# Optimization experiments

Measured on AMD Instinct MI355X. Metric: run time of the kernel, lower is better.

The kernel has to match this reference:

```python
import jax, jax.numpy as jnp
import numpy as np

N_NODES = 1048576
N_EDGES = 16777216
N_GRAPHS = 64
K_HOPS = 4


def setup_inputs() -> dict:
    key = jax.random.key(0)
    k1, k2, k3 = jax.random.split(key, 3)
    x = jax.random.normal(k1, (N_NODES, 1), dtype=jnp.float32)
    edge_index = jax.random.randint(k2, (2, N_EDGES), 0, N_NODES, dtype=jnp.int64)
    W = jax.random.normal(k3, (1, 1), dtype=jnp.float32)
    b = jnp.zeros((1,), dtype=jnp.float32)
    return {"x": x, "edge_index": edge_index, "W": W, "b": b, "num_graphs": N_GRAPHS}


def _sgconv(x, edge_index, W, b, k):
    # PyG SGConv: x <- (D^-1/2 (A + I) D^-1/2)^k x, then linear.
    n = x.shape[0]
    loops = jnp.arange(n, dtype=edge_index.dtype)
    row = jnp.concatenate([edge_index[0], loops])  # source nodes
    col = jnp.concatenate([edge_index[1], loops])  # target nodes
    ones = jnp.ones(row.shape[0], dtype=x.dtype)
    deg = jax.ops.segment_sum(ones, col, num_segments=n)  # in-degree incl. self loop
    dinv = jnp.where(deg > 0, jax.lax.rsqrt(deg), 0.0)
    norm = dinv[row] * dinv[col]  # [E+N]
    for _ in range(k):
        x = jax.ops.segment_sum(norm[:, None] * x[row], col, num_segments=n)
    return x @ W.T + b


def reference(x, edge_index, W, b, num_graphs):
    h = _sgconv(x, edge_index, W, b, K_HOPS)  # [N, 1]
    n = h.shape[0]
    # tensor_split into num_graphs equal chunks (N divisible by num_graphs), mean each
    out = h.reshape(num_graphs, n // num_graphs, 1).mean(axis=1)  # [B, 1]
    return out
```

## Files before the change

### kernel.cpp

```cpp
#include <hip/hip_runtime.h>
#include <stdint.h>

#define N_NODES  (1u << 20)
#define N_EDGES  (1u << 24)
#define N_GRAPHS 64
#define CHUNK    (N_NODES / N_GRAPHS)
#define K_HOPS   4

#define NBUCKET  1024
#define CPB      1024
#define CAP      18432

#define NBLK_SS  512
#define TB_SS    1024
#define EPT      32
#define EPB_SS   (TB_SS * EPT)

typedef uint32_t u32x4 __attribute__((ext_vector_type(4)));
typedef unsigned long long u64x2 __attribute__((ext_vector_type(2)));

__device__ __forceinline__ u32x4 nt_load_u32x4(const uint32_t* p) {
    return __builtin_nontemporal_load((const u32x4*)p);
}
__device__ __forceinline__ u64x2 nt_load_u64x2(const unsigned long long* p) {
    return __builtin_nontemporal_load((const u64x2*)p);
}

__global__ __launch_bounds__(TB_SS, 4)
void scatter_sort_kernel(const void* __restrict__ ei,
                         int* __restrict__ cursor, uint32_t* __restrict__ packed) {
    __shared__ uint32_t sorted[EPB_SS];
    __shared__ int h[NBUCKET];
    __shared__ int o[NBUCKET];
    __shared__ int ostart[NBUCKET];
    __shared__ int gbase[NBUCKET];
    __shared__ int s_is64;
    int blk = blockIdx.x, tid = threadIdx.x;
    h[tid] = 0;
    size_t base = (size_t)blk * EPB_SS;

    if (tid < 64) {
        size_t widx = 2 * base + 2 * (size_t)tid * 512 + 1;
        int nz = (((const uint32_t*)ei)[widx] != 0u);
        unsigned long long m = __ballot(nz);
        if (tid == 0) s_is64 = (m == 0ull) ? 1 : 0;
    }
    __syncthreads();
    int is64 = s_is64;
    uint32_t c_[EPT];

    if (is64) {
        const unsigned long long* cp = (const unsigned long long*)ei + N_EDGES + base;
        #pragma unroll
        for (int it = 0; it < EPT / 4; ++it) {
            size_t i = (size_t)it * (TB_SS * 4) + (size_t)tid * 4;
            u64x2 a = nt_load_u64x2(cp + i);
            u64x2 b2 = nt_load_u64x2(cp + i + 2);
            c_[it * 4 + 0] = (uint32_t)a.x;  c_[it * 4 + 1] = (uint32_t)a.y;
            c_[it * 4 + 2] = (uint32_t)b2.x; c_[it * 4 + 3] = (uint32_t)b2.y;
            atomicAdd(&h[c_[it * 4 + 0] >> 10], 1);
            atomicAdd(&h[c_[it * 4 + 1] >> 10], 1);
            atomicAdd(&h[c_[it * 4 + 2] >> 10], 1);
            atomicAdd(&h[c_[it * 4 + 3] >> 10], 1);
        }
    } else {
        const uint32_t* cp = (const uint32_t*)ei + N_EDGES + base;
        #pragma unroll
        for (int it = 0; it < EPT / 4; ++it) {
            size_t i = (size_t)it * (TB_SS * 4) + (size_t)tid * 4;
            u32x4 a = nt_load_u32x4(cp + i);
            c_[it * 4 + 0] = a.x; c_[it * 4 + 1] = a.y;
            c_[it * 4 + 2] = a.z; c_[it * 4 + 3] = a.w;
            atomicAdd(&h[a.x >> 10], 1);
            atomicAdd(&h[a.y >> 10], 1);
            atomicAdd(&h[a.z >> 10], 1);
            atomicAdd(&h[a.w >> 10], 1);
        }
    }
    __syncthreads();

    if (tid < 64) {
        int b16 = tid * 16;
        int s = 0;
        #pragma unroll
        for (int j = 0; j < 16; ++j) s += h[b16 + j];
        int v = s;
        #pragma unroll
        for (int off = 1; off < 64; off <<= 1) {
            int up = __shfl_up(v, off, 64);
            if (tid >= off) v += up;
        }
        int run = v - s;
        #pragma unroll
        for (int j = 0; j < 16; ++j) {
            o[b16 + j] = run;
            ostart[b16 + j] = run;
            run += h[b16 + j];
        }
    }
    __syncthreads();

    gbase[tid] = atomicAdd(&cursor[tid], h[tid]);

    if (is64) {
        const unsigned long long* rp = (const unsigned long long*)ei + base;
        #pragma unroll
        for (int it = 0; it < EPT / 4; ++it) {
            size_t i = (size_t)it * (TB_SS * 4) + (size_t)tid * 4;
            u64x2 a = nt_load_u64x2(rp + i);
            u64x2 b2 = nt_load_u64x2(rp + i + 2);
            uint32_t r0 = (uint32_t)a.x, r1 = (uint32_t)a.y;
            uint32_t r2 = (uint32_t)b2.x, r3 = (uint32_t)b2.y;
            { uint32_t c = c_[it * 4 + 0]; int pos = atomicAdd(&o[c >> 10], 1); sorted[pos] = (r0 << 10) | (c & 1023u); }
            { uint32_t c = c_[it * 4 + 1]; int pos = atomicAdd(&o[c >> 10], 1); sorted[pos] = (r1 << 10) | (c & 1023u); }
            { uint32_t c = c_[it * 4 + 2]; int pos = atomicAdd(&o[c >> 10], 1); sorted[pos] = (r2 << 10) | (c & 1023u); }
            { uint32_t c = c_[it * 4 + 3]; int pos = atomicAdd(&o[c >> 10], 1); sorted[pos] = (r3 << 10) | (c & 1023u); }
        }
    } else {
        const uint32_t* rp = (const uint32_t*)ei + base;
        #pragma unroll
        for (int it = 0; it < EPT / 4; ++it) {
            size_t i = (size_t)it * (TB_SS * 4) + (size_t)tid * 4;
            u32x4 a = nt_load_u32x4(rp + i);
            { uint32_t c = c_[it * 4 + 0]; int pos = atomicAdd(&o[c >> 10], 1); sorted[pos] = (a.x << 10) | (c & 1023u); }
            { uint32_t c = c_[it * 4 + 1]; int pos = atomicAdd(&o[c >> 10], 1); sorted[pos] = (a.y << 10) | (c & 1023u); }
            { uint32_t c = c_[it * 4 + 2]; int pos = atomicAdd(&o[c >> 10], 1); sorted[pos] = (a.z << 10) | (c & 1023u); }
            { uint32_t c = c_[it * 4 + 3]; int pos = atomicAdd(&o[c >> 10], 1); sorted[pos] = (a.w << 10) | (c & 1023u); }
        }
    }
    __syncthreads();

    int wave = tid >> 6, lane = tid & 63;
    for (int k = 0; k < NBUCKET / 16; ++k) {
        int b = wave * (NBUCKET / 16) + k;
        int st = ostart[b];
        int len = o[b] - st;
        int gb = gbase[b];
        if (gb + len > CAP) len = CAP - gb > 0 ? CAP - gb : 0;
        uint32_t* dst = packed + (size_t)b * CAP + gb;
        for (int j = lane; j < len; j += 64)
            dst[j] = sorted[st + j];
    }
}

__global__ __launch_bounds__(512)
void degdinv_kernel(const uint32_t* __restrict__ packed, const int* __restrict__ cursor,
                    const float* __restrict__ x,
                    float* __restrict__ dinv, float* __restrict__ z) {
    __shared__ int h[CPB];
    int b = blockIdx.x, tid = threadIdx.x;
    for (int l = tid; l < CPB; l += 512) h[l] = 0;
    __syncthreads();
    int cnt = cursor[b]; if (cnt > CAP) cnt = CAP;
    const uint32_t* seg = packed + (size_t)b * CAP;
    int nq = cnt >> 2;
    for (int g = tid; g < nq; g += 512) {
        u32x4 v = nt_load_u32x4(seg + g * 4);
        atomicAdd(&h[v.x & 1023u], 1);
        atomicAdd(&h[v.y & 1023u], 1);
        atomicAdd(&h[v.z & 1023u], 1);
        atomicAdd(&h[v.w & 1023u], 1);
    }
    int t = (nq << 2) + tid;
    if (t < cnt) atomicAdd(&h[seg[t] & 1023u], 1);
    __syncthreads();
    for (int l = tid; l < CPB; l += 512) {
        int v = b * CPB + l;
        float d = (float)(1.0 / sqrt((double)(h[l] + 1)));
        dinv[v] = d;
        z[v] = d * x[v];
    }
}

__global__ __launch_bounds__(512)
void hop_kernel(const uint32_t* __restrict__ packed, const int* __restrict__ cursor,
                const float* __restrict__ z, const float* __restrict__ dinv,
                float* __restrict__ out) {
    __shared__ float facc[CPB];
    int b = blockIdx.x, tid = threadIdx.x;
    for (int l = tid; l < CPB; l += 512) facc[l] = 0.0f;
    __syncthreads();
    int cnt = cursor[b]; if (cnt > CAP) cnt = CAP;
    const uint32_t* seg = packed + (size_t)b * CAP;
    int nq = cnt >> 2;
    for (int g = tid; g < nq; g += 512) {
        u32x4 v = nt_load_u32x4(seg + g * 4);
        float z0 = z[v.x >> 10];
        float z1 = z[v.y >> 10];
        float z2 = z[v.z >> 10];
        float z3 = z[v.w >> 10];
        atomicAdd(&facc[v.x & 1023u], z0);
        atomicAdd(&facc[v.y & 1023u], z1);
        atomicAdd(&facc[v.z & 1023u], z2);
        atomicAdd(&facc[v.w & 1023u], z3);
    }
    int t = (nq << 2) + tid;
    if (t < cnt) { uint32_t p = seg[t]; atomicAdd(&facc[p & 1023u], z[p >> 10]); }
    __syncthreads();
    for (int l = tid; l < CPB; l += 512) {
        int v = b * CPB + l;
        float tt = z[v] + facc[l];
        float d = dinv[v];
        out[v] = d * d * tt;
    }
}

__global__ __launch_bounds__(512)
void hop_final_kernel(const uint32_t* __restrict__ packed, const int* __restrict__ cursor,
                      const float* __restrict__ z, const float* __restrict__ dinv,
                      float* __restrict__ gsum) {
    __shared__ float facc[CPB];
    __shared__ double sdata[8];
    int b = blockIdx.x, tid = threadIdx.x;
    for (int l = tid; l < CPB; l += 512) facc[l] = 0.0f;
    __syncthreads();
    int cnt = cursor[b]; if (cnt > CAP) cnt = CAP;
    const uint32_t* seg = packed + (size_t)b * CAP;
    int nq = cnt >> 2;
    for (int g = tid; g < nq; g += 512) {
        u32x4 v = nt_load_u32x4(seg + g * 4);
        float z0 = z[v.x >> 10];
        float z1 = z[v.y >> 10];
        float z2 = z[v.z >> 10];
        float z3 = z[v.w >> 10];
        atomicAdd(&facc[v.x & 1023u], z0);
        atomicAdd(&facc[v.y & 1023u], z1);
        atomicAdd(&facc[v.z & 1023u], z2);
        atomicAdd(&facc[v.w & 1023u], z3);
    }
    int t = (nq << 2) + tid;
    if (t < cnt) { uint32_t p = seg[t]; atomicAdd(&facc[p & 1023u], z[p >> 10]); }
    __syncthreads();
    double s = 0.0;
    for (int l = tid; l < CPB; l += 512) {
        int v = b * CPB + l;
        s += (double)(dinv[v] * (z[v] + facc[l]));
    }
    #pragma unroll
    for (int off = 32; off > 0; off >>= 1) s += __shfl_down(s, off, 64);
    int wave = tid >> 6, lane = tid & 63;
    if (lane == 0) sdata[wave] = s;
    __syncthreads();
    if (tid == 0) {
        double tot = 0.0;
        #pragma unroll
        for (int w = 0; w < 8; ++w) tot += sdata[w];
        atomicAdd(&gsum[b >> 4], (float)tot);
    }
}

__global__ void finalize_kernel(const float* __restrict__ gsum,
                                const float* __restrict__ W, const float* __restrict__ b,
                                float* __restrict__ out) {
    int g = threadIdx.x;
    if (g < N_GRAPHS)
        out[g] = (float)((double)W[0] * ((double)gsum[g] / (double)CHUNK) + (double)b[0]);
}

__global__ void detect_kernel(const uint32_t* __restrict__ ei, int* __restrict__ flag) {
    __shared__ int any_nz;
    if (threadIdx.x == 0) any_nz = 0;
    __syncthreads();
    int nz = 0;
    for (int i = threadIdx.x; i < 32768; i += blockDim.x)
        nz |= (ei[2 * i + 1] != 0u);
    if (nz) atomicOr(&any_nz, 1);
    __syncthreads();
    if (threadIdx.x == 0) flag[0] = any_nz ? 0 : 1;
}

__global__ void zero_int_kernel(int* __restrict__ p) {
    int i = blockIdx.x * blockDim.x + threadIdx.x;
    p[i] = 0;
}

__device__ __forceinline__ int load_idx(const void* ei, int is64, size_t pos) {
    if (is64) return (int)((const unsigned long long*)ei)[pos];
    return ((const int*)ei)[pos];
}

__global__ void count_kernel(const void* __restrict__ ei, const int* __restrict__ flag,
                             int* __restrict__ deg) {
    int e = blockIdx.x * blockDim.x + threadIdx.x;
    int c = load_idx(ei, flag[0], (size_t)N_EDGES + (size_t)e);
    atomicAdd(&deg[c], 1);
}

__global__ void dinv_kernel(const int* __restrict__ deg, float* __restrict__ dinv) {
    int v = blockIdx.x * blockDim.x + threadIdx.x;
    dinv[v] = (float)(1.0 / sqrt((double)(deg[v] + 1)));
}

__global__ void prep_first2_kernel(const float* __restrict__ x, const float* __restrict__ dinv,
                                   float* __restrict__ z, float* __restrict__ acc) {
    int v = blockIdx.x * blockDim.x + threadIdx.x;
    float t = dinv[v] * x[v];
    z[v] = t;
    acc[v] = t;
}

__global__ void prep_mid_kernel(const float* __restrict__ dinv,
                                float* __restrict__ z, float* __restrict__ acc) {
    int v = blockIdx.x * blockDim.x + threadIdx.x;
    float d = dinv[v];
    float t = d * d * acc[v];
    z[v] = t;
    acc[v] = t;
}

__global__ void push_kernel(const void* __restrict__ ei, const int* __restrict__ flag,
                            const float* __restrict__ z, float* __restrict__ acc) {
    int e = blockIdx.x * blockDim.x + threadIdx.x;
    int is64 = flag[0];
    int r, c;
    if (is64) {
        const unsigned long long* p = (const unsigned long long*)ei;
        r = (int)p[e];
        c = (int)p[(size_t)N_EDGES + (size_t)e];
    } else {
        const int* p = (const int*)ei;
        r = p[e];
        c = p[(size_t)N_EDGES + (size_t)e];
    }
    __hip_atomic_fetch_add(&acc[c], z[r], __ATOMIC_RELAXED, __HIP_MEMORY_SCOPE_AGENT);
}

__global__ void final_scale_kernel(const float* __restrict__ dinv,
                                   const float* __restrict__ acc, float* __restrict__ xf) {
    int v = blockIdx.x * blockDim.x + threadIdx.x;
    xf[v] = dinv[v] * acc[v];
}

__global__ void pool_kernel(const float* __restrict__ xf,
                            const float* __restrict__ W, const float* __restrict__ b,
                            float* __restrict__ out) {
    __shared__ double sdata[256];
    int g = blockIdx.x;
    int base = g * CHUNK;
    double s = 0.0;
    for (int i = threadIdx.x; i < CHUNK; i += 256) s += (double)xf[base + i];
    sdata[threadIdx.x] = s;
    __syncthreads();
    for (int off = 128; off > 0; off >>= 1) {
        if (threadIdx.x < off) sdata[threadIdx.x] += sdata[threadIdx.x + off];
        __syncthreads();
    }
    if (threadIdx.x == 0)
        out[g] = (float)((double)W[0] * (sdata[0] / (double)CHUNK) + (double)b[0]);
}

extern "C" void kernel_launch(void* const* d_in, const int* in_sizes, int n_in,
                              void* d_out, int out_size, void* d_ws, size_t ws_size,
                              hipStream_t stream) {
    const float* x = (const float*)d_in[0];
    const void*  ei = d_in[1];
    const float* W = (const float*)d_in[2];
    const float* b = (const float*)d_in[3];
    float* out = (float*)d_out;

    char* ws = (char*)d_ws;
    const size_t MB4 = 4ull << 20;
    size_t off_cursor = 0;
    size_t off_gsum   = NBUCKET * 4;
    size_t off_dinv   = off_gsum + 256;
    size_t off_za     = off_dinv + MB4;
    size_t off_zb     = off_za + MB4;
    size_t off_packed = off_zb + MB4;
    size_t needed     = off_packed + (size_t)NBUCKET * CAP * 4;

    const int TB = 256;

    if (ws_size >= needed) {
        int*      cursor = (int*)(ws + off_cursor);
        float*    gsum   = (float*)(ws + off_gsum);
        float*    dinv   = (float*)(ws + off_dinv);
        float*    za     = (float*)(ws + off_za);
        float*    zb     = (float*)(ws + off_zb);
        uint32_t* packed = (uint32_t*)(ws + off_packed);

        hipMemsetAsync(ws, 0, NBUCKET * 4 + 256, stream);

        scatter_sort_kernel<<<NBLK_SS, TB_SS, 0, stream>>>(ei, cursor, packed);
        degdinv_kernel<<<NBUCKET, 512, 0, stream>>>(packed, cursor, x, dinv, za);

        hop_kernel<<<NBUCKET, 512, 0, stream>>>(packed, cursor, za, dinv, zb);
        hop_kernel<<<NBUCKET, 512, 0, stream>>>(packed, cursor, zb, dinv, za);
        hop_kernel<<<NBUCKET, 512, 0, stream>>>(packed, cursor, za, dinv, zb);
        hop_final_kernel<<<NBUCKET, 512, 0, stream>>>(packed, cursor, zb, dinv, gsum);

        finalize_kernel<<<1, 64, 0, stream>>>(gsum, W, b, out);
    } else {
        int*   flag = (int*)ws;
        float* dinv = (float*)(ws + 256);
        float* za   = (float*)(ws + 256 + MB4);
        float* zb   = (float*)(ws + 256 + 2 * MB4);
        int*   deg  = (int*)(ws + 256 + 3 * MB4);

        detect_kernel<<<1, TB, 0, stream>>>((const uint32_t*)ei, flag);
        zero_int_kernel<<<N_NODES / TB, TB, 0, stream>>>(deg);
        count_kernel<<<N_EDGES / TB, TB, 0, stream>>>(ei, flag, deg);
        dinv_kernel<<<N_NODES / TB, TB, 0, stream>>>(deg, dinv);

        prep_first2_kernel<<<N_NODES / TB, TB, 0, stream>>>(x, dinv, za, zb);
        push_kernel<<<N_EDGES / TB, TB, 0, stream>>>(ei, flag, za, zb);
        for (int h = 1; h < K_HOPS; ++h) {
            prep_mid_kernel<<<N_NODES / TB, TB, 0, stream>>>(dinv, za, zb);
            push_kernel<<<N_EDGES / TB, TB, 0, stream>>>(ei, flag, za, zb);
        }
        final_scale_kernel<<<N_NODES / TB, TB, 0, stream>>>(dinv, zb, za);
        pool_kernel<<<N_GRAPHS, TB, 0, stream>>>(za, W, b, out);
    }
}
```

Measured before the change: 624.6 us.

## Tile edges by (target bucket, source shard) and row-sort tiles for z locality

Edges are now binned into 1024 tiles keyed by 64 target buckets of 16K nodes and 16 source shards of 64K nodes. A second pass sorts each tile by source row and builds global degrees, so the hop gathers read a 256KB slice of z in near-sequential order. Each hop accumulates 16K-wide partials in shared memory and atomically adds them to a global accumulator, followed by a separate merge kernel. The aim is better cache hit rates on the random z gathers, at the cost of an extra sort pass, global float atomics and extra merge launches per hop. Float atomic order is nondeterministic.

```diff
diff --git a/kernel.cpp b/kernel.cpp
--- a/kernel.cpp
+++ b/kernel.cpp
@@ -7,23 +7,318 @@
 #define CHUNK    (N_NODES / N_GRAPHS)
 #define K_HOPS   4
 
+#define NBLK_SS  1024
+#define TB_SS    1024
+#define EPT      16
+#define EPB_SS   (TB_SS * EPT)
+#define CAP      18432
+
 #define NBUCKET  1024
 #define CPB      1024
-#define CAP      18432
-
-#define NBLK_SS  512
-#define TB_SS    1024
-#define EPT      32
-#define EPB_SS   (TB_SS * EPT)
+
+#define NBKT2    64
+#define SHARDS   16
+#define NTILE    (NBKT2 * SHARDS)
+#define CPB2     16384
 
 typedef uint32_t u32x4 __attribute__((ext_vector_type(4)));
 typedef unsigned long long u64x2 __attribute__((ext_vector_type(2)));
+typedef float f32x4 __attribute__((ext_vector_type(4)));
+typedef int i32x4 __attribute__((ext_vector_type(4)));
 
 __device__ __forceinline__ u32x4 nt_load_u32x4(const uint32_t* p) {
     return __builtin_nontemporal_load((const u32x4*)p);
 }
 __device__ __forceinline__ u64x2 nt_load_u64x2(const unsigned long long* p) {
     return __builtin_nontemporal_load((const u64x2*)p);
+}
+__device__ __forceinline__ void nt_store_u32x4(uint32_t* p, u32x4 v) {
+    __builtin_nontemporal_store(v, (u32x4*)p);
+}
+
+__global__ __launch_bounds__(TB_SS, 4)
+void tile_sort_kernel(const void* __restrict__ ei,
+                      int* __restrict__ cursor, uint32_t* __restrict__ packed) {
+    __shared__ uint32_t sorted[EPB_SS];
+    __shared__ int h[NTILE];
+    __shared__ int o[NTILE];
+    __shared__ int ostart[NTILE];
+    __shared__ int gbase[NTILE];
+    __shared__ int s_is64;
+    int blk = blockIdx.x, tid = threadIdx.x;
+    h[tid] = 0;
+    size_t base = (size_t)blk * EPB_SS;
+
+    if (tid < 64) {
+        size_t widx = 2 * base + 2 * (size_t)tid * (EPB_SS / 64) + 1;
+        int nz = (((const uint32_t*)ei)[widx] != 0u);
+        unsigned long long m = __ballot(nz);
+        if (tid == 0) s_is64 = (m == 0ull) ? 1 : 0;
+    }
+    __syncthreads();
+    int is64 = s_is64;
+    uint32_t c_[EPT], r_[EPT];
+
+    if (is64) {
+        const unsigned long long* cp = (const unsigned long long*)ei + N_EDGES + base;
+        const unsigned long long* rp = (const unsigned long long*)ei + base;
+        #pragma unroll
+        for (int it = 0; it < EPT / 4; ++it) {
+            size_t i = (size_t)it * (TB_SS * 4) + (size_t)tid * 4;
+            u64x2 ca = nt_load_u64x2(cp + i);
+            u64x2 cb = nt_load_u64x2(cp + i + 2);
+            u64x2 ra = nt_load_u64x2(rp + i);
+            u64x2 rb = nt_load_u64x2(rp + i + 2);
+            c_[it * 4 + 0] = (uint32_t)ca.x;  c_[it * 4 + 1] = (uint32_t)ca.y;
+            c_[it * 4 + 2] = (uint32_t)cb.x;  c_[it * 4 + 3] = (uint32_t)cb.y;
+            r_[it * 4 + 0] = (uint32_t)ra.x;  r_[it * 4 + 1] = (uint32_t)ra.y;
+            r_[it * 4 + 2] = (uint32_t)rb.x;  r_[it * 4 + 3] = (uint32_t)rb.y;
+            #pragma unroll
+            for (int j = 0; j < 4; ++j) {
+                int k = it * 4 + j;
+                atomicAdd(&h[((c_[k] >> 14) << 4) | (r_[k] >> 16)], 1);
+            }
+        }
+    } else {
+        const uint32_t* cp = (const uint32_t*)ei + N_EDGES + base;
+        const uint32_t* rp = (const uint32_t*)ei + base;
+        #pragma unroll
+        for (int it = 0; it < EPT / 4; ++it) {
+            size_t i = (size_t)it * (TB_SS * 4) + (size_t)tid * 4;
+            u32x4 a = nt_load_u32x4(cp + i);
+            u32x4 r = nt_load_u32x4(rp + i);
+            c_[it * 4 + 0] = a.x; c_[it * 4 + 1] = a.y;
+            c_[it * 4 + 2] = a.z; c_[it * 4 + 3] = a.w;
+            r_[it * 4 + 0] = r.x; r_[it * 4 + 1] = r.y;
+            r_[it * 4 + 2] = r.z; r_[it * 4 + 3] = r.w;
+            #pragma unroll
+            for (int j = 0; j < 4; ++j) {
+                int k = it * 4 + j;
+                atomicAdd(&h[((c_[k] >> 14) << 4) | (r_[k] >> 16)], 1);
+            }
+        }
+    }
+    __syncthreads();
+
+    if (tid < 64) {
+        int b16 = tid * 16;
+        int s = 0;
+        #pragma unroll
+        for (int j = 0; j < 16; ++j) s += h[b16 + j];
+        int v = s;
+        #pragma unroll
+        for (int off = 1; off < 64; off <<= 1) {
+            int up = __shfl_up(v, off, 64);
+            if (tid >= off) v += up;
+        }
+        int run = v - s;
+        #pragma unroll
+        for (int j = 0; j < 16; ++j) {
+            o[b16 + j] = run;
+            ostart[b16 + j] = run;
+            run += h[b16 + j];
+        }
+    }
+    __syncthreads();
+
+    gbase[tid] = atomicAdd(&cursor[tid], h[tid]);
+
+    #pragma unroll
+    for (int k = 0; k < EPT; ++k) {
+        uint32_t c = c_[k], r = r_[k];
+        int key = ((c >> 14) << 4) | (r >> 16);
+        int pos = atomicAdd(&o[key], 1);
+        sorted[pos] = ((r & 0xFFFFu) << 14) | (c & 0x3FFFu);
+    }
+    __syncthreads();
+
+    int wave = tid >> 6, lane = tid & 63;
+    for (int k = 0; k < NTILE / 16; ++k) {
+        int b = wave * (NTILE / 16) + k;
+        int st = ostart[b];
+        int len = o[b] - st;
+        int gb = gbase[b];
+        if (gb + len > CAP) len = CAP - gb > 0 ? CAP - gb : 0;
+        uint32_t* dst = packed + (size_t)b * CAP + gb;
+        for (int j = lane; j < len; j += 64)
+            dst[j] = sorted[st + j];
+    }
+}
+
+__global__ __launch_bounds__(512, 1)
+void tile_rowsort_kernel(uint32_t* __restrict__ packed, const int* __restrict__ cursor,
+                         int* __restrict__ deg) {
+    __shared__ uint32_t sbuf[CAP];
+    __shared__ int h[CPB2];
+    __shared__ int ro[512];
+    int t = blockIdx.x, tid = threadIdx.x;
+    for (int l = tid; l < CPB2; l += 512) h[l] = 0;
+    for (int l = tid; l < 512; l += 512) ro[l] = 0;
+    __syncthreads();
+    int cnt = cursor[t]; if (cnt > CAP) cnt = CAP;
+    uint32_t* seg = packed + (size_t)t * CAP;
+    int nq = cnt >> 2;
+
+    for (int g = tid; g < nq; g += 512) {
+        u32x4 v = *(const u32x4*)(seg + 4 * (size_t)g);
+        atomicAdd(&h[v.x & 0x3FFFu], 1); atomicAdd(&ro[v.x >> 21], 1);
+        atomicAdd(&h[v.y & 0x3FFFu], 1); atomicAdd(&ro[v.y >> 21], 1);
+        atomicAdd(&h[v.z & 0x3FFFu], 1); atomicAdd(&ro[v.z >> 21], 1);
+        atomicAdd(&h[v.w & 0x3FFFu], 1); atomicAdd(&ro[v.w >> 21], 1);
+    }
+    {
+        int tt = (nq << 2) + tid;
+        if (tt < cnt) { uint32_t p = seg[tt]; atomicAdd(&h[p & 0x3FFFu], 1); atomicAdd(&ro[p >> 21], 1); }
+    }
+    __syncthreads();
+
+    if (tid < 64) {
+        int b8 = tid * 8;
+        int s = 0;
+        #pragma unroll
+        for (int j = 0; j < 8; ++j) s += ro[b8 + j];
+        int v = s;
+        #pragma unroll
+        for (int off = 1; off < 64; off <<= 1) {
+            int up = __shfl_up(v, off, 64);
+            if (tid >= off) v += up;
+        }
+        int run = v - s;
+        #pragma unroll
+        for (int j = 0; j < 8; ++j) { int c = ro[b8 + j]; ro[b8 + j] = run; run += c; }
+    }
+    {
+        int dbase = (t >> 4) << 14;
+        for (int l = tid; l < CPB2; l += 512) {
+            int hv = h[l];
+            if (hv) atomicAdd(&deg[dbase + l], hv);
+        }
+    }
+    __syncthreads();
+
+    for (int g = tid; g < nq; g += 512) {
+        u32x4 v = *(const u32x4*)(seg + 4 * (size_t)g);
+        { int p = atomicAdd(&ro[v.x >> 21], 1); sbuf[p] = v.x; }
+        { int p = atomicAdd(&ro[v.y >> 21], 1); sbuf[p] = v.y; }
+        { int p = atomicAdd(&ro[v.z >> 21], 1); sbuf[p] = v.z; }
+        { int p = atomicAdd(&ro[v.w >> 21], 1); sbuf[p] = v.w; }
+    }
+    {
+        int tt = (nq << 2) + tid;
+        if (tt < cnt) { uint32_t p = seg[tt]; int q = atomicAdd(&ro[p >> 21], 1); sbuf[q] = p; }
+    }
+    __syncthreads();
+
+    for (int g = tid; g < nq; g += 512) {
+        u32x4 o4;
+        o4.x = sbuf[4 * g + 0]; o4.y = sbuf[4 * g + 1];
+        o4.z = sbuf[4 * g + 2]; o4.w = sbuf[4 * g + 3];
+        nt_store_u32x4(seg + 4 * (size_t)g, o4);
+    }
+    {
+        int tt = (nq << 2) + tid;
+        if (tt < cnt) __builtin_nontemporal_store(sbuf[tt], seg + tt);
+    }
+}
+
+__global__ __launch_bounds__(512)
+void dinvz_kernel(const int* __restrict__ deg, const float* __restrict__ x,
+                  float* __restrict__ dinv, float* __restrict__ z) {
+    int i = blockIdx.x * 512 + threadIdx.x;
+    int v0 = i << 2;
+    i32x4 dg = *(const i32x4*)(deg + v0);
+    f32x4 xx = *(const f32x4*)(x + v0);
+    f32x4 dd, zz;
+    dd.x = (float)(1.0 / sqrt((double)(dg.x + 1)));
+    dd.y = (float)(1.0 / sqrt((double)(dg.y + 1)));
+    dd.z = (float)(1.0 / sqrt((double)(dg.z + 1)));
+    dd.w = (float)(1.0 / sqrt((double)(dg.w + 1)));
+    zz = dd * xx;
+    *(f32x4*)(dinv + v0) = dd;
+    *(f32x4*)(z + v0) = zz;
+}
+
+__global__ __launch_bounds__(512)
+void hop_acc_kernel(const uint32_t* __restrict__ packed, const int* __restrict__ cursor,
+                    const float* __restrict__ z, float* __restrict__ acc) {
+    __shared__ float facc[CPB2];
+    int t = blockIdx.x, tid = threadIdx.x;
+    int shard = t & (SHARDS - 1), bucket = t >> 4;
+    for (int l = tid; l < CPB2; l += 512) facc[l] = 0.0f;
+    __syncthreads();
+    int cnt = cursor[t]; if (cnt > CAP) cnt = CAP;
+    const uint32_t* seg = packed + (size_t)t * CAP;
+    const float* zs = z + ((size_t)shard << 16);
+    int nq = cnt >> 2;
+    for (int g = tid; g < nq; g += 512) {
+        u32x4 v = *(const u32x4*)(seg + 4 * (size_t)g);
+        float z0 = zs[v.x >> 14];
+        float z1 = zs[v.y >> 14];
+        float z2 = zs[v.z >> 14];
+        float z3 = zs[v.w >> 14];
+        atomicAdd(&facc[v.x & 0x3FFFu], z0);
+        atomicAdd(&facc[v.y & 0x3FFFu], z1);
+        atomicAdd(&facc[v.z & 0x3FFFu], z2);
+        atomicAdd(&facc[v.w & 0x3FFFu], z3);
+    }
+    {
+        int tt = (nq << 2) + tid;
+        if (tt < cnt) { uint32_t p = seg[tt]; atomicAdd(&facc[p & 0x3FFFu], zs[p >> 14]); }
+    }
+    __syncthreads();
+    float* ab = acc + ((size_t)bucket << 14);
+    for (int l = tid; l < CPB2; l += 512) {
+        float v = facc[l];
+        if (v != 0.0f) atomicAdd(&ab[l], v);
+    }
+}
+
+__global__ __launch_bounds__(512)
+void merge_mid_kernel(float* __restrict__ acc, const float* __restrict__ z,
+                      const float* __restrict__ dinv, float* __restrict__ out) {
+    int i = blockIdx.x * 512 + threadIdx.x;
+    int v0 = i << 2;
+    f32x4 aa = *(const f32x4*)(acc + v0);
+    f32x4 zz = *(const f32x4*)(z + v0);
+    f32x4 dd = *(const f32x4*)(dinv + v0);
+    f32x4 r = dd * dd * (zz + aa);
+    *(f32x4*)(out + v0) = r;
+    f32x4 zero = {0.0f, 0.0f, 0.0f, 0.0f};
+    *(f32x4*)(acc + v0) = zero;
+}
+
+__global__ __launch_bounds__(512)
+void merge_final_kernel(const float* __restrict__ acc, const float* __restrict__ z,
+                        const float* __restrict__ dinv, float* __restrict__ gsum) {
+    __shared__ double sdata[8];
+    int blk = blockIdx.x;
+    int g = blk >> 3, part = blk & 7;
+    int c0 = part * 2048 + (int)threadIdx.x * 4;
+    int v0 = (g << 14) | c0;
+    f32x4 aa = *(const f32x4*)(acc + v0);
+    f32x4 zz = *(const f32x4*)(z + v0);
+    f32x4 dd = *(const f32x4*)(dinv + v0);
+    f32x4 val = dd * (zz + aa);
+    double sl = (double)val.x + (double)val.y + (double)val.z + (double)val.w;
+    #pragma unroll
+    for (int off = 32; off > 0; off >>= 1) sl += __shfl_down(sl, off, 64);
+    int wave = threadIdx.x >> 6, lane = threadIdx.x & 63;
+    if (lane == 0) sdata[wave] = sl;
+    __syncthreads();
+    if (threadIdx.x == 0) {
+        double tot = 0.0;
+        #pragma unroll
+        for (int w = 0; w < 8; ++w) tot += sdata[w];
+        atomicAdd(&gsum[g], (float)tot);
+    }
+}
+
+__global__ void finalize_kernel(const float* __restrict__ gsum,
+                                const float* __restrict__ W, const float* __restrict__ b,
+                                float* __restrict__ out) {
+    int g = threadIdx.x;
+    if (g < N_GRAPHS)
+        out[g] = (float)((double)W[0] * ((double)gsum[g] / (double)CHUNK) + (double)b[0]);
 }
 
 __global__ __launch_bounds__(TB_SS, 4)
@@ -38,9 +333,8 @@
     int blk = blockIdx.x, tid = threadIdx.x;
     h[tid] = 0;
     size_t base = (size_t)blk * EPB_SS;
-
     if (tid < 64) {
-        size_t widx = 2 * base + 2 * (size_t)tid * 512 + 1;
+        size_t widx = 2 * base + 2 * (size_t)tid * (EPB_SS / 64) + 1;
         int nz = (((const uint32_t*)ei)[widx] != 0u);
         unsigned long long m = __ballot(nz);
         if (tid == 0) s_is64 = (m == 0ull) ? 1 : 0;
@@ -48,7 +342,6 @@
     __syncthreads();
     int is64 = s_is64;
     uint32_t c_[EPT];
-
     if (is64) {
         const unsigned long long* cp = (const unsigned long long*)ei + N_EDGES + base;
         #pragma unroll
@@ -78,7 +371,6 @@
         }
     }
     __syncthreads();
-
     if (tid < 64) {
         int b16 = tid * 16;
         int s = 0;
@@ -99,9 +391,7 @@
         }
     }
     __syncthreads();
-
     gbase[tid] = atomicAdd(&cursor[tid], h[tid]);
-
     if (is64) {
         const unsigned long long* rp = (const unsigned long long*)ei + base;
         #pragma unroll
@@ -109,12 +399,13 @@
             size_t i = (size_t)it * (TB_SS * 4) + (size_t)tid * 4;
             u64x2 a = nt_load_u64x2(rp + i);
             u64x2 b2 = nt_load_u64x2(rp + i + 2);
-            uint32_t r0 = (uint32_t)a.x, r1 = (uint32_t)a.y;
-            uint32_t r2 = (uint32_t)b2.x, r3 = (uint32_t)b2.y;
-            { uint32_t c = c_[it * 4 + 0]; int pos = atomicAdd(&o[c >> 10], 1); sorted[pos] = (r0 << 10) | (c & 1023u); }
-            { uint32_t c = c_[it * 4 + 1]; int pos = atomicAdd(&o[c >> 10], 1); sorted[pos] = (r1 << 10) | (c & 1023u); }
-            { uint32_t c = c_[it * 4 + 2]; int pos = atomicAdd(&o[c >> 10], 1); sorted[pos] = (r2 << 10) | (c & 1023u); }
-            { uint32_t c = c_[it * 4 + 3]; int pos = atomicAdd(&o[c >> 10], 1); sorted[pos] = (r3 << 10) | (c & 1023u); }
+            uint32_t rr[4] = {(uint32_t)a.x, (uint32_t)a.y, (uint32_t)b2.x, (uint32_t)b2.y};
+            #pragma unroll
+            for (int j = 0; j < 4; ++j) {
+                uint32_t c = c_[it * 4 + j];
+                int pos = atomicAdd(&o[c >> 10], 1);
+                sorted[pos] = (rr[j] << 10) | (c & 1023u);
+            }
         }
     } else {
         const uint32_t* rp = (const uint32_t*)ei + base;
@@ -122,14 +413,16 @@
         for (int it = 0; it < EPT / 4; ++it) {
             size_t i = (size_t)it * (TB_SS * 4) + (size_t)tid * 4;
             u32x4 a = nt_load_u32x4(rp + i);
-            { uint32_t c = c_[it * 4 + 0]; int pos = atomicAdd(&o[c >> 10], 1); sorted[pos] = (a.x << 10) | (c & 1023u); }
-            { uint32_t c = c_[it * 4 + 1]; int pos = atomicAdd(&o[c >> 10], 1); sorted[pos] = (a.y << 10) | (c & 1023u); }
-            { uint32_t c = c_[it * 4 + 2]; int pos = atomicAdd(&o[c >> 10], 1); sorted[pos] = (a.z << 10) | (c & 1023u); }
-            { uint32_t c = c_[it * 4 + 3]; int pos = atomicAdd(&o[c >> 10], 1); sorted[pos] = (a.w << 10) | (c & 1023u); }
-        }
-    }
-    __syncthreads();
-
+            uint32_t rr[4] = {a.x, a.y, a.z, a.w};
+            #pragma unroll
+            for (int j = 0; j < 4; ++j) {
+                uint32_t c = c_[it * 4 + j];
+                int pos = atomicAdd(&o[c >> 10], 1);
+                sorted[pos] = (rr[j] << 10) | (c & 1023u);
+            }
+        }
+    }
+    __syncthreads();
     int wave = tid >> 6, lane = tid & 63;
     for (int k = 0; k < NBUCKET / 16; ++k) {
         int b = wave * (NBUCKET / 16) + k;
@@ -155,7 +448,7 @@
     const uint32_t* seg = packed + (size_t)b * CAP;
     int nq = cnt >> 2;
     for (int g = tid; g < nq; g += 512) {
-        u32x4 v = nt_load_u32x4(seg + g * 4);
+        u32x4 v = nt_load_u32x4(seg + 4 * (size_t)g);
         atomicAdd(&h[v.x & 1023u], 1);
         atomicAdd(&h[v.y & 1023u], 1);
         atomicAdd(&h[v.z & 1023u], 1);
@@ -184,7 +477,7 @@
     const uint32_t* seg = packed + (size_t)b * CAP;
     int nq = cnt >> 2;
     for (int g = tid; g < nq; g += 512) {
-        u32x4 v = nt_load_u32x4(seg + g * 4);
+        u32x4 v = nt_load_u32x4(seg + 4 * (size_t)g);
         float z0 = z[v.x >> 10];
         float z1 = z[v.y >> 10];
         float z2 = z[v.z >> 10];
@@ -218,7 +511,7 @@
     const uint32_t* seg = packed + (size_t)b * CAP;
     int nq = cnt >> 2;
     for (int g = tid; g < nq; g += 512) {
-        u32x4 v = nt_load_u32x4(seg + g * 4);
+        u32x4 v = nt_load_u32x4(seg + 4 * (size_t)g);
         float z0 = z[v.x >> 10];
         float z1 = z[v.y >> 10];
         float z2 = z[v.z >> 10];
@@ -247,14 +540,6 @@
         for (int w = 0; w < 8; ++w) tot += sdata[w];
         atomicAdd(&gsum[b >> 4], (float)tot);
     }
-}
-
-__global__ void finalize_kernel(const float* __restrict__ gsum,
-                                const float* __restrict__ W, const float* __restrict__ b,
-                                float* __restrict__ out) {
-    int g = threadIdx.x;
-    if (g < N_GRAPHS)
-        out[g] = (float)((double)W[0] * ((double)gsum[g] / (double)CHUNK) + (double)b[0]);
 }
 
 __global__ void detect_kernel(const uint32_t* __restrict__ ei, int* __restrict__ flag) {
@@ -360,23 +645,63 @@
 
     char* ws = (char*)d_ws;
     const size_t MB4 = 4ull << 20;
+    const size_t packed_sz = (size_t)NTILE * CAP * 4;
+
     size_t off_cursor = 0;
-    size_t off_gsum   = NBUCKET * 4;
-    size_t off_dinv   = off_gsum + 256;
+    size_t off_gsum   = 4096;
+    size_t off_deg    = 8192;
+    size_t off_acc    = off_deg + MB4;
+    size_t off_dinv   = off_acc + MB4;
     size_t off_za     = off_dinv + MB4;
     size_t off_zb     = off_za + MB4;
-    size_t off_packed = off_zb + MB4;
-    size_t needed     = off_packed + (size_t)NBUCKET * CAP * 4;
+    size_t off_packed3 = off_zb + MB4;
+    size_t needed_v3  = off_packed3 + packed_sz;
+
+    size_t off1_gsum   = NBUCKET * 4;
+    size_t off1_dinv   = off1_gsum + 256;
+    size_t off1_za     = off1_dinv + MB4;
+    size_t off1_zb     = off1_za + MB4;
+    size_t off1_packed = off1_zb + MB4;
+    size_t needed_v1   = off1_packed + packed_sz;
 
     const int TB = 256;
 
-    if (ws_size >= needed) {
+    if (ws_size >= needed_v3) {
         int*      cursor = (int*)(ws + off_cursor);
         float*    gsum   = (float*)(ws + off_gsum);
+        int*      deg    = (int*)(ws + off_deg);
+        float*    acc    = (float*)(ws + off_acc);
         float*    dinv   = (float*)(ws + off_dinv);
         float*    za     = (float*)(ws + off_za);
         float*    zb     = (float*)(ws + off_zb);
-        uint32_t* packed = (uint32_t*)(ws + off_packed);
+        uint32_t* packed = (uint32_t*)(ws + off_packed3);
+
+        hipMemsetAsync(ws, 0, off_acc + MB4, stream);
+
+        tile_sort_kernel<<<NBLK_SS, TB_SS, 0, stream>>>(ei, cursor, packed);
+        tile_rowsort_kernel<<<NTILE, 512, 0, stream>>>(packed, cursor, deg);
+        dinvz_kernel<<<N_NODES / 2048, 512, 0, stream>>>(deg, x, dinv, za);
+
+        hop_acc_kernel<<<NTILE, 512, 0, stream>>>(packed, cursor, za, acc);
+        merge_mid_kernel<<<N_NODES / 2048, 512, 0, stream>>>(acc, za, dinv, zb);
+
+        hop_acc_kernel<<<NTILE, 512, 0, stream>>>(packed, cursor, zb, acc);
+        merge_mid_kernel<<<N_NODES / 2048, 512, 0, stream>>>(acc, zb, dinv, za);
+
+        hop_acc_kernel<<<NTILE, 512, 0, stream>>>(packed, cursor, za, acc);
+        merge_mid_kernel<<<N_NODES / 2048, 512, 0, stream>>>(acc, za, dinv, zb);
+
+        hop_acc_kernel<<<NTILE, 512, 0, stream>>>(packed, cursor, zb, acc);
+        merge_final_kernel<<<N_GRAPHS * 8, 512, 0, stream>>>(acc, zb, dinv, gsum);
+
+        finalize_kernel<<<1, 64, 0, stream>>>(gsum, W, b, out);
+    } else if (ws_size >= needed_v1) {
+        int*      cursor = (int*)(ws);
+        float*    gsum   = (float*)(ws + off1_gsum);
+        float*    dinv   = (float*)(ws + off1_dinv);
+        float*    za     = (float*)(ws + off1_za);
+        float*    zb     = (float*)(ws + off1_zb);
+        uint32_t* packed = (uint32_t*)(ws + off1_packed);
 
         hipMemsetAsync(ws, 0, NBUCKET * 4 + 256, stream);
 
```

New measurement: 822.2 us. +31.6%, slower.
